# Kernel tuning notes

Measured on AMD Instinct MI355X. Metric: run time of the kernel, lower is better.

The kernel has to match this reference:

```python
import jax, jax.numpy as jnp
import numpy as np

H = 4096
L_CAND = 4

def setup_inputs() -> dict:
    key = jax.random.key(0)
    ks = jax.random.split(key, 8)
    s = 1.0 / np.sqrt(H)
    L = jax.random.uniform(ks[0], (L_CAND, H, H), minval=-s, maxval=s, dtype=jnp.float32)
    R = jax.random.uniform(ks[1], (L_CAND, H, H), minval=-s, maxval=s, dtype=jnp.float32)
    b = jnp.zeros((L_CAND, 1, H), dtype=jnp.float32)
    # candidate 3 is initialized to identity / zero bias in the torch module
    L = L.at[3].set(jnp.eye(H, dtype=jnp.float32))
    R = R.at[3].set(jnp.eye(H, dtype=jnp.float32))
    W_score = jax.random.uniform(ks[2], (H, 1), minval=-s, maxval=s, dtype=jnp.float32)
    x = jax.random.normal(ks[3], (1, H), dtype=jnp.float32)
    h_prev = jax.random.normal(ks[4], (1, H), dtype=jnp.float32)
    return {"x": x, "h_prev": h_prev, "L": L, "R": R, "b": b, "W_score": W_score}

def reference(x, h_prev, L, R, b, W_score):
    def score_mix(lst):
        # lst: [l, 1, H] candidates -> softmax-weighted mixture + argmax + margin
        s = jnp.einsum('lbh,ho->l', lst, W_score)          # [l]
        w = jax.nn.softmax(s)
        out = jnp.einsum('l,lbh->bh', w, lst)              # [1, H]
        top2 = jax.lax.top_k(s, 2)[0]
        return out, jnp.argmax(s), top2[0] - top2[1]

    mmL = lambda v: jnp.einsum('bh,lhk->lbk', v, L)        # batched [1,H]x[H,H] over l=4
    mmR = lambda v: jnp.einsum('bh,lhk->lbk', v, R)

    xL, hL, hR = mmL(x), mmL(h_prev), mmR(h_prev)
    z_1 = jax.nn.sigmoid(xL[0] + hR[0] + b[0])
    r   = jax.nn.sigmoid(xL[1] + hR[1] + b[1])
    z_2 = jax.nn.sigmoid(xL[0] + hR[0] + b[0])             # same as z_1 in source

    rh, i0, m0 = score_mix(hL * mmR(r) + b)
    h_tilde, i1, m1 = score_mix(jnp.tanh(xL + mmR(rh) + b))
    oneMinusZ1, i2, m2 = score_mix(1.0 - (mmR(z_1) + b))
    zh_tilde, i3, m3 = score_mix(mmL(h_tilde) * mmR(oneMinusZ1) + b)
    z2h, i4, m4 = score_mix(hL * mmR(z_2) + b)
    h_next, i5, m5 = score_mix(mmL(zh_tilde) + mmR(z2h) + b)

    G_structure = jnp.concatenate([jnp.array([0, 1, 0]),
                                   jnp.stack([i0, i1, i2, i3, i4, i5])])
    margins = jnp.stack([m0, m1, m2, m3, m4, m5])
    return h_next, G_structure, margins
```

## Files before the change

kernel.cpp:

```cpp
#include <hip/hip_runtime.h>
#include <hip/hip_fp16.h>

#define H 4096


template<int NV>
__global__ __launch_bounds__(256) void gemv_f32_k(const float* __restrict__ M,
                                                  const float* __restrict__ V0,
                                                  const float* __restrict__ V1,
                                                  float* __restrict__ out,
                                                  __half* __restrict__ M16) {
  int b = blockIdx.x;
  const int hc = b & 63;
  const int kt = (b >> 6) & 3;
  const int l  = b >> 8;
  const int tid = threadIdx.x;
  const int k0 = kt * 1024 + tid * 4;
  const int h0 = hc * 64;

  __shared__ float vs[NV * 64];
  if (tid < 64) vs[tid] = V0[h0 + tid];
  if (NV > 1 && tid >= 64 && tid < 128) vs[tid] = V1[h0 + tid - 64];
  __syncthreads();

  const size_t base = ((size_t)l * H + h0) * H + k0;
  const float* Mp = M + base;
  __half* M16p = M16 + base;

  float acc[NV][4];
#pragma unroll
  for (int v = 0; v < NV; ++v)
#pragma unroll
    for (int j = 0; j < 4; ++j) acc[v][j] = 0.0f;

#pragma unroll 2
  for (int hh = 0; hh < 64; ++hh) {
    float4 m = *reinterpret_cast<const float4*>(Mp + (size_t)hh * H);
    __half t[4] = {__float2half(m.x), __float2half(m.y),
                   __float2half(m.z), __float2half(m.w)};
    *reinterpret_cast<uint2*>(M16p + (size_t)hh * H) =
        *reinterpret_cast<const uint2*>(t);
#pragma unroll
    for (int v = 0; v < NV; ++v) {
      const float s = vs[v * 64 + hh];
      acc[v][0] = fmaf(s, m.x, acc[v][0]);
      acc[v][1] = fmaf(s, m.y, acc[v][1]);
      acc[v][2] = fmaf(s, m.z, acc[v][2]);
      acc[v][3] = fmaf(s, m.w, acc[v][3]);
    }
  }
#pragma unroll
  for (int v = 0; v < NV; ++v)
#pragma unroll
    for (int j = 0; j < 4; ++j)
      atomicAdd(out + ((size_t)(v * 3 + l)) * H + k0 + j, acc[v][j]);
}

template<int NV, bool MIX>
__global__ __launch_bounds__(256) void gemv_f16_k(
    const __half* __restrict__ M, const float* __restrict__ vecbase,
    const float* __restrict__ scores, int sbase,
    float* __restrict__ out, float* __restrict__ mixstore,
    int os0, int os1, int os2, float* __restrict__ dout) {
  int b = blockIdx.x;
  const int hc = b & 63;
  const int kt = (b >> 6) & 1;
  const int l  = b >> 7;
  const int tid = threadIdx.x;
  const int k0 = kt * 2048 + tid * 8;
  const int h0 = hc * 64;

  __shared__ float vs[NV * 64];
  if (MIX) {
    const bool storeblk = (l == 0 && kt == 0);
    if (tid < 64) {
#pragma unroll
      for (int v = 0; v < NV; ++v) {
        const float* sc = scores + (size_t)(sbase + v) * 4;
        float s0 = sc[0], s1 = sc[1], s2 = sc[2], s3 = sc[3];
        float mx = fmaxf(fmaxf(s0, s1), fmaxf(s2, s3));
        float e0 = expf(s0 - mx), e1 = expf(s1 - mx);
        float e2 = expf(s2 - mx), e3 = expf(s3 - mx);
        float inv = 1.0f / (e0 + e1 + e2 + e3);
        const float* cb = vecbase + (size_t)v * 4 * H + h0 + tid;
        float m = (e0 * cb[0] + e1 * cb[H] + e2 * cb[2 * H] + e3 * cb[3 * H]) * inv;
        vs[v * 64 + tid] = m;
        if (storeblk) mixstore[(size_t)v * H + h0 + tid] = m;
      }
    }
    if (storeblk && hc == 0 && tid == 0) {
      const int os[3] = {os0, os1, os2};
#pragma unroll
      for (int v = 0; v < NV; ++v) {
        const float* sc = scores + (size_t)(sbase + v) * 4;
        float s[4] = {sc[0], sc[1], sc[2], sc[3]};
        int idx = 0; float mx = s[0];
        for (int q = 1; q < 4; ++q) if (s[q] > mx) { mx = s[q]; idx = q; }
        float second = -1e30f;
        for (int q = 0; q < 4; ++q) if (q != idx && s[q] > second) second = s[q];
        dout[H + 3 + os[v]] = (float)idx;
        dout[H + 9 + os[v]] = mx - second;
      }
    }
  } else {
    for (int i = tid; i < NV * 64; i += 256)
      vs[i] = vecbase[(size_t)(i >> 6) * H + h0 + (i & 63)];
  }
  __syncthreads();

  const __half* Mp = M + ((size_t)l * H + h0) * H + k0;

  float acc[NV][8];
#pragma unroll
  for (int v = 0; v < NV; ++v)
#pragma unroll
    for (int j = 0; j < 8; ++j) acc[v][j] = 0.0f;

#pragma unroll 2
  for (int hh = 0; hh < 64; ++hh) {
    union { uint4 u; __half2 h2[4]; } cv;
    cv.u = *reinterpret_cast<const uint4*>(Mp + (size_t)hh * H);
    float fr[8];
#pragma unroll
    for (int j = 0; j < 4; ++j) {
      float2 t = __half22float2(cv.h2[j]);
      fr[2 * j] = t.x; fr[2 * j + 1] = t.y;
    }
#pragma unroll
    for (int v = 0; v < NV; ++v) {
      const float s = vs[v * 64 + hh];
#pragma unroll
      for (int j = 0; j < 8; ++j) acc[v][j] = fmaf(s, fr[j], acc[v][j]);
    }
  }
#pragma unroll
  for (int v = 0; v < NV; ++v)
#pragma unroll
    for (int j = 0; j < 8; ++j)
      atomicAdd(out + ((size_t)(v * 3 + l)) * H + k0 + j, acc[v][j]);
}

__device__ __forceinline__ float sigmoidf_(float x) {
  return 1.0f / (1.0f + expf(-x));
}

__global__ __launch_bounds__(256) void zr_k(float* __restrict__ f,
                                            const float* __restrict__ bias) {
  const int h = blockIdx.x * 256 + threadIdx.x;
  f[56 * H + h] = sigmoidf_(f[0 * H + h] + f[6 * H + h] + bias[h]);
  f[55 * H + h] = sigmoidf_(f[1 * H + h] + f[7 * H + h] + bias[H + h]);
}

template<int NW>
__device__ __forceinline__ void reduce_atomic(float* vals, float* sc, int tid) {
  __shared__ float red[4][NW];
  const int lane = tid & 63, wv = tid >> 6;
#pragma unroll
  for (int j = 0; j < NW; ++j) {
    float v = vals[j];
#pragma unroll
    for (int off = 32; off > 0; off >>= 1) v += __shfl_down(v, off);
    if (lane == 0) red[wv][j] = v;
  }
  __syncthreads();
  if (tid < NW)
    atomicAdd(sc + tid, red[0][tid] + red[1][tid] + red[2][tid] + red[3][tid]);
}

__global__ __launch_bounds__(256) void cs2_k(float* __restrict__ f,
                                             const float* __restrict__ hprev,
                                             const float* __restrict__ bias,
                                             const float* __restrict__ Ws) {
  const int h = blockIdx.x * 256 + threadIdx.x;
  const int tid = threadIdx.x;
  const float hp = hprev[h];
  const float r3 = f[55 * H + h], z3 = f[56 * H + h];
  const float ws = Ws[h];
  float crh[4], com[4], cz2[4];
#pragma unroll
  for (int l = 0; l < 3; ++l) {
    const float hl = f[(3 + l) * H + h];
    const float rr = f[(9 + l) * H + h];
    const float zz = f[(12 + l) * H + h];
    const float bl = bias[(size_t)l * H + h];
    crh[l] = fmaf(hl, rr, bl);
    com[l] = 1.0f - (zz + bl);
    cz2[l] = fmaf(hl, zz, bl);
  }
  {
    const float bl = bias[(size_t)3 * H + h];
    crh[3] = fmaf(hp, r3, bl);
    com[3] = 1.0f - (z3 + bl);
    cz2[3] = fmaf(hp, z3, bl);
  }
#pragma unroll
  for (int l = 0; l < 4; ++l) {
    f[(31 + l) * H + h] = crh[l];
    f[(35 + l) * H + h] = com[l];
    f[(39 + l) * H + h] = cz2[l];
  }
  float vals[12];
#pragma unroll
  for (int l = 0; l < 4; ++l) {
    vals[l]     = crh[l] * ws;
    vals[4 + l] = com[l] * ws;
    vals[8 + l] = cz2[l] * ws;
  }
  reduce_atomic<12>(vals, f + 30 * H, tid);
}

#define OP_MUL  0
#define OP_TANH 1
#define OP_ADD  2

template<int OP>
__global__ __launch_bounds__(256) void csx_k(const float* __restrict__ A,
                                             const float* __restrict__ A3,
                                             const float* __restrict__ B,
                                             const float* __restrict__ B3,
                                             const float* __restrict__ bias,
                                             const float* __restrict__ Ws,
                                             float* __restrict__ cand,
                                             float* __restrict__ sc) {
  const int h = blockIdx.x * 256 + threadIdx.x;
  const int tid = threadIdx.x;
  const float ws = Ws[h];
  float c[4];
#pragma unroll
  for (int l = 0; l < 4; ++l) {
    const float a = (l < 3) ? A[(size_t)l * H + h] : A3[h];
    const float b = (l < 3) ? B[(size_t)l * H + h] : B3[h];
    const float bl = bias[(size_t)l * H + h];
    if (OP == OP_MUL)  c[l] = fmaf(a, b, bl);
    if (OP == OP_TANH) c[l] = tanhf(a + b + bl);
    if (OP == OP_ADD)  c[l] = a + b + bl;
    cand[(size_t)l * H + h] = c[l];
  }
  float vals[4] = {c[0] * ws, c[1] * ws, c[2] * ws, c[3] * ws};
  reduce_atomic<4>(vals, sc, tid);
}

__global__ __launch_bounds__(256) void final_k(const float* __restrict__ f,
                                               float* __restrict__ dout) {
  const int h = blockIdx.x * 256 + threadIdx.x;
  const float* sc = f + 30 * H + 5 * 4;
  float s0 = sc[0], s1 = sc[1], s2 = sc[2], s3 = sc[3];
  float mx = fmaxf(fmaxf(s0, s1), fmaxf(s2, s3));
  float e0 = expf(s0 - mx), e1 = expf(s1 - mx);
  float e2 = expf(s2 - mx), e3 = expf(s3 - mx);
  float inv = 1.0f / (e0 + e1 + e2 + e3);
  const float* cb = f + 51 * H + h;
  dout[h] = (e0 * cb[0] + e1 * cb[H] + e2 * cb[2 * H] + e3 * cb[3 * H]) * inv;
  if (blockIdx.x == 0 && threadIdx.x == 0) {
    float s[4] = {s0, s1, s2, s3};
    int idx = 0; float m = s[0];
    for (int q = 1; q < 4; ++q) if (s[q] > m) { m = s[q]; idx = q; }
    float second = -1e30f;
    for (int q = 0; q < 4; ++q) if (q != idx && s[q] > second) second = s[q];
    dout[H + 0] = 0.f; dout[H + 1] = 1.f; dout[H + 2] = 0.f;
    dout[H + 3 + 5] = (float)idx;
    dout[H + 9 + 5] = m - second;
  }
}

extern "C" void kernel_launch(void* const* d_in, const int* in_sizes, int n_in,
                              void* d_out, int out_size, void* d_ws, size_t ws_size,
                              hipStream_t stream) {
  const float* x  = (const float*)d_in[0];
  const float* hp = (const float*)d_in[1];
  const float* L  = (const float*)d_in[2];
  const float* R  = (const float*)d_in[3];
  const float* bb = (const float*)d_in[4];
  const float* Ws = (const float*)d_in[5];
  float* out = (float*)d_out;

  __half* L16 = (__half*)d_ws;
  __half* R16 = L16 + (size_t)3 * H * H;
  float*  f   = (float*)(R16 + (size_t)3 * H * H);
  float*  sc  = f + 30 * H;

  hipMemsetAsync(f, 0, (size_t)31 * H * sizeof(float), stream);

  gemv_f32_k<2><<<768, 256, 0, stream>>>(L, x, hp, f, L16);
  gemv_f32_k<1><<<768, 256, 0, stream>>>(R, hp, nullptr, f + 6 * H, R16);

  zr_k<<<16, 256, 0, stream>>>(f, bb);

  gemv_f16_k<2, false><<<384, 256, 0, stream>>>(R16, f + 55 * H, nullptr, 0,
                                                f + 9 * H, nullptr, 0, 0, 0, nullptr);
  cs2_k<<<16, 256, 0, stream>>>(f, hp, bb, Ws);

  gemv_f16_k<3, true><<<384, 256, 0, stream>>>(R16, f + 31 * H, sc, 0,
                                               f + 15 * H, f + 57 * H, 0, 2, 4, out);
  csx_k<OP_TANH><<<16, 256, 0, stream>>>(f, x, f + 15 * H, f + 57 * H,
                                         bb, Ws, f + 43 * H, sc + 12);

  gemv_f16_k<1, true><<<384, 256, 0, stream>>>(L16, f + 43 * H, sc, 3,
                                               f + 24 * H, f + 60 * H, 1, 0, 0, out);
  csx_k<OP_MUL><<<16, 256, 0, stream>>>(f + 24 * H, f + 60 * H, f + 18 * H,
                                        f + 58 * H, bb, Ws, f + 47 * H, sc + 16);

  gemv_f16_k<1, true><<<384, 256, 0, stream>>>(L16, f + 47 * H, sc, 4,
                                               f + 27 * H, f + 61 * H, 3, 0, 0, out);
  csx_k<OP_ADD><<<16, 256, 0, stream>>>(f + 27 * H, f + 61 * H, f + 21 * H,
                                        f + 59 * H, bb, Ws, f + 51 * H, sc + 20);

  final_k<<<16, 256, 0, stream>>>(f, out);
}
```

Measured before the change: 796.6 us.

## Fuse all GRU stages into one persistent kernel with grid barriers

Replaces the sequence of gemv and elementwise launches with a single persistent kernel of 768 blocks that runs every stage, separated by a hierarchical atomic grid barrier. Workspace zeroing moves inside the kernel and tile shapes change (128-row fp32 tiles, 32-row fp16 tiles). The aim is to remove launch overhead and inter-kernel gaps. In exchange it relies on all blocks being co-resident, adds barrier spin costs, and doubles the atomic traffic in the fp16 phases.

```diff
diff --git a/kernel.cpp b/kernel.cpp
--- a/kernel.cpp
+++ b/kernel.cpp
@@ -4,23 +4,84 @@
 #define H 4096
 
 
+__device__ __forceinline__ float sigmoidf_(float x) {
+  return 1.0f / (1.0f + expf(-x));
+}
+
+__device__ __forceinline__ void soft4(const float* sc, float* w) {
+  float s0 = sc[0], s1 = sc[1], s2 = sc[2], s3 = sc[3];
+  float mx = fmaxf(fmaxf(s0, s1), fmaxf(s2, s3));
+  float e0 = expf(s0 - mx), e1 = expf(s1 - mx);
+  float e2 = expf(s2 - mx), e3 = expf(s3 - mx);
+  float inv = 1.0f / (e0 + e1 + e2 + e3);
+  w[0] = e0 * inv; w[1] = e1 * inv; w[2] = e2 * inv; w[3] = e3 * inv;
+}
+
+__device__ __forceinline__ void idxmargin(const float* sc, float* dout, int os) {
+  float s[4] = {sc[0], sc[1], sc[2], sc[3]};
+  int idx = 0; float mx = s[0];
+  for (int q = 1; q < 4; ++q) if (s[q] > mx) { mx = s[q]; idx = q; }
+  float second = -1e30f;
+  for (int q = 0; q < 4; ++q) if (q != idx && s[q] > second) second = s[q];
+  dout[H + 3 + os] = (float)idx;
+  dout[H + 9 + os] = mx - second;
+}
+
+__device__ __forceinline__ void gridbar(int* bar) {
+  __syncthreads();
+  __threadfence();
+  if (threadIdx.x == 0) {
+    int* gen  = bar;
+    int* root = bar + 16;
+    int* gcnt = bar + 32 + (blockIdx.x >> 6) * 16;
+    int g = __hip_atomic_load(gen, __ATOMIC_RELAXED, __HIP_MEMORY_SCOPE_AGENT);
+    bool done = false;
+    if (atomicAdd(gcnt, 1) == 63) {
+      atomicExch(gcnt, 0);
+      if (atomicAdd(root, 1) == 11) {
+        atomicExch(root, 0);
+        atomicAdd(gen, 1);
+        done = true;
+      }
+    }
+    if (!done) {
+      while (__hip_atomic_load(gen, __ATOMIC_RELAXED,
+                               __HIP_MEMORY_SCOPE_AGENT) == g)
+        __builtin_amdgcn_s_sleep(4);
+    }
+  }
+  __syncthreads();
+  __threadfence();
+}
+
+template<int NW>
+__device__ __forceinline__ void reduce_atomic(float* vals, float* scdst, int tid) {
+  __shared__ float red[4][12];
+  const int lane = tid & 63, wv = tid >> 6;
+#pragma unroll
+  for (int j = 0; j < NW; ++j) {
+    float v = vals[j];
+#pragma unroll
+    for (int off = 32; off > 0; off >>= 1) v += __shfl_down(v, off);
+    if (lane == 0) red[wv][j] = v;
+  }
+  __syncthreads();
+  if (tid < NW)
+    atomicAdd(scdst + tid, red[0][tid] + red[1][tid] + red[2][tid] + red[3][tid]);
+}
+
 template<int NV>
-__global__ __launch_bounds__(256) void gemv_f32_k(const float* __restrict__ M,
-                                                  const float* __restrict__ V0,
-                                                  const float* __restrict__ V1,
-                                                  float* __restrict__ out,
-                                                  __half* __restrict__ M16) {
-  int b = blockIdx.x;
-  const int hc = b & 63;
-  const int kt = (b >> 6) & 3;
-  const int l  = b >> 8;
+__device__ void phase_gemv32(const float* __restrict__ M,
+                             const float* __restrict__ V0,
+                             const float* __restrict__ V1,
+                             float* __restrict__ fout,
+                             __half* __restrict__ M16, int task, float* smem) {
+  const int hc = task & 31, kt = (task >> 5) & 3, l = task >> 7;
   const int tid = threadIdx.x;
   const int k0 = kt * 1024 + tid * 4;
-  const int h0 = hc * 64;
-
-  __shared__ float vs[NV * 64];
-  if (tid < 64) vs[tid] = V0[h0 + tid];
-  if (NV > 1 && tid >= 64 && tid < 128) vs[tid] = V1[h0 + tid - 64];
+  const int h0 = hc * 128;
+  if (tid < 128) smem[tid] = V0[h0 + tid];
+  else if (NV > 1) smem[tid] = V1[h0 + tid - 128];
   __syncthreads();
 
   const size_t base = ((size_t)l * H + h0) * H + k0;
@@ -33,8 +94,8 @@
 #pragma unroll
     for (int j = 0; j < 4; ++j) acc[v][j] = 0.0f;
 
-#pragma unroll 2
-  for (int hh = 0; hh < 64; ++hh) {
+#pragma unroll 4
+  for (int hh = 0; hh < 128; ++hh) {
     float4 m = *reinterpret_cast<const float4*>(Mp + (size_t)hh * H);
     __half t[4] = {__float2half(m.x), __float2half(m.y),
                    __float2half(m.z), __float2half(m.w)};
@@ -42,7 +103,7 @@
         *reinterpret_cast<const uint2*>(t);
 #pragma unroll
     for (int v = 0; v < NV; ++v) {
-      const float s = vs[v * 64 + hh];
+      const float s = smem[v * 128 + hh];
       acc[v][0] = fmaf(s, m.x, acc[v][0]);
       acc[v][1] = fmaf(s, m.y, acc[v][1]);
       acc[v][2] = fmaf(s, m.z, acc[v][2]);
@@ -53,71 +114,20 @@
   for (int v = 0; v < NV; ++v)
 #pragma unroll
     for (int j = 0; j < 4; ++j)
-      atomicAdd(out + ((size_t)(v * 3 + l)) * H + k0 + j, acc[v][j]);
-}
-
-template<int NV, bool MIX>
-__global__ __launch_bounds__(256) void gemv_f16_k(
-    const __half* __restrict__ M, const float* __restrict__ vecbase,
-    const float* __restrict__ scores, int sbase,
-    float* __restrict__ out, float* __restrict__ mixstore,
-    int os0, int os1, int os2, float* __restrict__ dout) {
-  int b = blockIdx.x;
-  const int hc = b & 63;
-  const int kt = (b >> 6) & 1;
-  const int l  = b >> 7;
-  const int tid = threadIdx.x;
-  const int k0 = kt * 2048 + tid * 8;
-  const int h0 = hc * 64;
-
-  __shared__ float vs[NV * 64];
-  if (MIX) {
-    const bool storeblk = (l == 0 && kt == 0);
-    if (tid < 64) {
-#pragma unroll
-      for (int v = 0; v < NV; ++v) {
-        const float* sc = scores + (size_t)(sbase + v) * 4;
-        float s0 = sc[0], s1 = sc[1], s2 = sc[2], s3 = sc[3];
-        float mx = fmaxf(fmaxf(s0, s1), fmaxf(s2, s3));
-        float e0 = expf(s0 - mx), e1 = expf(s1 - mx);
-        float e2 = expf(s2 - mx), e3 = expf(s3 - mx);
-        float inv = 1.0f / (e0 + e1 + e2 + e3);
-        const float* cb = vecbase + (size_t)v * 4 * H + h0 + tid;
-        float m = (e0 * cb[0] + e1 * cb[H] + e2 * cb[2 * H] + e3 * cb[3 * H]) * inv;
-        vs[v * 64 + tid] = m;
-        if (storeblk) mixstore[(size_t)v * H + h0 + tid] = m;
-      }
-    }
-    if (storeblk && hc == 0 && tid == 0) {
-      const int os[3] = {os0, os1, os2};
-#pragma unroll
-      for (int v = 0; v < NV; ++v) {
-        const float* sc = scores + (size_t)(sbase + v) * 4;
-        float s[4] = {sc[0], sc[1], sc[2], sc[3]};
-        int idx = 0; float mx = s[0];
-        for (int q = 1; q < 4; ++q) if (s[q] > mx) { mx = s[q]; idx = q; }
-        float second = -1e30f;
-        for (int q = 0; q < 4; ++q) if (q != idx && s[q] > second) second = s[q];
-        dout[H + 3 + os[v]] = (float)idx;
-        dout[H + 9 + os[v]] = mx - second;
-      }
-    }
-  } else {
-    for (int i = tid; i < NV * 64; i += 256)
-      vs[i] = vecbase[(size_t)(i >> 6) * H + h0 + (i & 63)];
-  }
-  __syncthreads();
-
-  const __half* Mp = M + ((size_t)l * H + h0) * H + k0;
-
+      atomicAdd(fout + (size_t)(v * 3 + l) * H + k0 + j, acc[v][j]);
+}
+
+template<int NV>
+__device__ void dot16(const __half* __restrict__ Mp, const float* __restrict__ vs,
+                      float* __restrict__ fout, int l, int k0) {
   float acc[NV][8];
 #pragma unroll
   for (int v = 0; v < NV; ++v)
 #pragma unroll
     for (int j = 0; j < 8; ++j) acc[v][j] = 0.0f;
 
-#pragma unroll 2
-  for (int hh = 0; hh < 64; ++hh) {
+#pragma unroll 4
+  for (int hh = 0; hh < 32; ++hh) {
     union { uint4 u; __half2 h2[4]; } cv;
     cv.u = *reinterpret_cast<const uint4*>(Mp + (size_t)hh * H);
     float fr[8];
@@ -128,7 +138,7 @@
     }
 #pragma unroll
     for (int v = 0; v < NV; ++v) {
-      const float s = vs[v * 64 + hh];
+      const float s = vs[v * 32 + hh];
 #pragma unroll
       for (int j = 0; j < 8; ++j) acc[v][j] = fmaf(s, fr[j], acc[v][j]);
     }
@@ -137,129 +147,191 @@
   for (int v = 0; v < NV; ++v)
 #pragma unroll
     for (int j = 0; j < 8; ++j)
-      atomicAdd(out + ((size_t)(v * 3 + l)) * H + k0 + j, acc[v][j]);
-}
-
-__device__ __forceinline__ float sigmoidf_(float x) {
-  return 1.0f / (1.0f + expf(-x));
-}
-
-__global__ __launch_bounds__(256) void zr_k(float* __restrict__ f,
-                                            const float* __restrict__ bias) {
-  const int h = blockIdx.x * 256 + threadIdx.x;
-  f[56 * H + h] = sigmoidf_(f[0 * H + h] + f[6 * H + h] + bias[h]);
-  f[55 * H + h] = sigmoidf_(f[1 * H + h] + f[7 * H + h] + bias[H + h]);
-}
-
-template<int NW>
-__device__ __forceinline__ void reduce_atomic(float* vals, float* sc, int tid) {
-  __shared__ float red[4][NW];
-  const int lane = tid & 63, wv = tid >> 6;
-#pragma unroll
-  for (int j = 0; j < NW; ++j) {
-    float v = vals[j];
-#pragma unroll
-    for (int off = 32; off > 0; off >>= 1) v += __shfl_down(v, off);
-    if (lane == 0) red[wv][j] = v;
-  }
-  __syncthreads();
-  if (tid < NW)
-    atomicAdd(sc + tid, red[0][tid] + red[1][tid] + red[2][tid] + red[3][tid]);
-}
-
-__global__ __launch_bounds__(256) void cs2_k(float* __restrict__ f,
-                                             const float* __restrict__ hprev,
-                                             const float* __restrict__ bias,
-                                             const float* __restrict__ Ws) {
-  const int h = blockIdx.x * 256 + threadIdx.x;
+      atomicAdd(fout + (size_t)(v * 3 + l) * H + k0 + j, acc[v][j]);
+}
+
+__global__ __launch_bounds__(256, 3) void mega_k(
+    const float* __restrict__ x, const float* __restrict__ hp,
+    const float* __restrict__ L, const float* __restrict__ R,
+    const float* __restrict__ bias, const float* __restrict__ Ws,
+    float* __restrict__ dout, __half* __restrict__ L16,
+    __half* __restrict__ R16, float* __restrict__ f, int* __restrict__ bar) {
+  __shared__ float smem[256];
+  const int b = blockIdx.x;
   const int tid = threadIdx.x;
-  const float hp = hprev[h];
-  const float r3 = f[55 * H + h], z3 = f[56 * H + h];
-  const float ws = Ws[h];
-  float crh[4], com[4], cz2[4];
-#pragma unroll
-  for (int l = 0; l < 3; ++l) {
-    const float hl = f[(3 + l) * H + h];
-    const float rr = f[(9 + l) * H + h];
-    const float zz = f[(12 + l) * H + h];
-    const float bl = bias[(size_t)l * H + h];
-    crh[l] = fmaf(hl, rr, bl);
-    com[l] = 1.0f - (zz + bl);
-    cz2[l] = fmaf(hl, zz, bl);
-  }
+  float* sc = f + 30 * H;
+
+  for (int i = b * 256 + tid; i < 31 * H; i += 768 * 256) f[i] = 0.0f;
+  gridbar(bar);
+
+  if (b < 384) phase_gemv32<2>(L, x, hp, f, L16, b, smem);
+  else         phase_gemv32<1>(R, hp, nullptr, f + 6 * H, R16, b - 384, smem);
+  gridbar(bar);
+
   {
-    const float bl = bias[(size_t)3 * H + h];
-    crh[3] = fmaf(hp, r3, bl);
-    com[3] = 1.0f - (z3 + bl);
-    cz2[3] = fmaf(hp, z3, bl);
-  }
-#pragma unroll
-  for (int l = 0; l < 4; ++l) {
-    f[(31 + l) * H + h] = crh[l];
-    f[(35 + l) * H + h] = com[l];
-    f[(39 + l) * H + h] = cz2[l];
-  }
-  float vals[12];
-#pragma unroll
-  for (int l = 0; l < 4; ++l) {
-    vals[l]     = crh[l] * ws;
-    vals[4 + l] = com[l] * ws;
-    vals[8 + l] = cz2[l] * ws;
-  }
-  reduce_atomic<12>(vals, f + 30 * H, tid);
-}
-
-#define OP_MUL  0
-#define OP_TANH 1
-#define OP_ADD  2
-
-template<int OP>
-__global__ __launch_bounds__(256) void csx_k(const float* __restrict__ A,
-                                             const float* __restrict__ A3,
-                                             const float* __restrict__ B,
-                                             const float* __restrict__ B3,
-                                             const float* __restrict__ bias,
-                                             const float* __restrict__ Ws,
-                                             float* __restrict__ cand,
-                                             float* __restrict__ sc) {
-  const int h = blockIdx.x * 256 + threadIdx.x;
-  const int tid = threadIdx.x;
-  const float ws = Ws[h];
-  float c[4];
-#pragma unroll
-  for (int l = 0; l < 4; ++l) {
-    const float a = (l < 3) ? A[(size_t)l * H + h] : A3[h];
-    const float b = (l < 3) ? B[(size_t)l * H + h] : B3[h];
-    const float bl = bias[(size_t)l * H + h];
-    if (OP == OP_MUL)  c[l] = fmaf(a, b, bl);
-    if (OP == OP_TANH) c[l] = tanhf(a + b + bl);
-    if (OP == OP_ADD)  c[l] = a + b + bl;
-    cand[(size_t)l * H + h] = c[l];
-  }
-  float vals[4] = {c[0] * ws, c[1] * ws, c[2] * ws, c[3] * ws};
-  reduce_atomic<4>(vals, sc, tid);
-}
-
-__global__ __launch_bounds__(256) void final_k(const float* __restrict__ f,
-                                               float* __restrict__ dout) {
-  const int h = blockIdx.x * 256 + threadIdx.x;
-  const float* sc = f + 30 * H + 5 * 4;
-  float s0 = sc[0], s1 = sc[1], s2 = sc[2], s3 = sc[3];
-  float mx = fmaxf(fmaxf(s0, s1), fmaxf(s2, s3));
-  float e0 = expf(s0 - mx), e1 = expf(s1 - mx);
-  float e2 = expf(s2 - mx), e3 = expf(s3 - mx);
-  float inv = 1.0f / (e0 + e1 + e2 + e3);
-  const float* cb = f + 51 * H + h;
-  dout[h] = (e0 * cb[0] + e1 * cb[H] + e2 * cb[2 * H] + e3 * cb[3 * H]) * inv;
-  if (blockIdx.x == 0 && threadIdx.x == 0) {
-    float s[4] = {s0, s1, s2, s3};
-    int idx = 0; float m = s[0];
-    for (int q = 1; q < 4; ++q) if (s[q] > m) { m = s[q]; idx = q; }
-    float second = -1e30f;
-    for (int q = 0; q < 4; ++q) if (q != idx && s[q] > second) second = s[q];
-    dout[H + 0] = 0.f; dout[H + 1] = 1.f; dout[H + 2] = 0.f;
-    dout[H + 3 + 5] = (float)idx;
-    dout[H + 9 + 5] = m - second;
+    const int hc = b & 127, kt = (b >> 7) & 1, l = b >> 8;
+    const int h0 = hc * 32, k0 = kt * 2048 + tid * 8;
+    if (tid < 32) {
+      int row = h0 + tid;
+      smem[tid]      = sigmoidf_(f[1 * H + row] + f[7 * H + row] + bias[H + row]);
+      smem[32 + tid] = sigmoidf_(f[0 * H + row] + f[6 * H + row] + bias[row]);
+    }
+    __syncthreads();
+    dot16<2>(R16 + ((size_t)l * H + h0) * H + k0, smem, f + 9 * H, l, k0);
+  }
+  gridbar(bar);
+
+  if (b < 16) {
+    const int h = b * 256 + tid;
+    const float hpv = hp[h];
+    const float z3 = sigmoidf_(f[0 * H + h] + f[6 * H + h] + bias[h]);
+    const float r3 = sigmoidf_(f[1 * H + h] + f[7 * H + h] + bias[H + h]);
+    const float ws = Ws[h];
+    float vals[12];
+#pragma unroll
+    for (int l = 0; l < 3; ++l) {
+      const float hl = f[(3 + l) * H + h], rr = f[(9 + l) * H + h],
+                  zz = f[(12 + l) * H + h];
+      const float bl = bias[(size_t)l * H + h];
+      float crh = fmaf(hl, rr, bl), com = 1.0f - (zz + bl), cz2 = fmaf(hl, zz, bl);
+      f[(size_t)(31 + l) * H + h] = crh;
+      f[(size_t)(35 + l) * H + h] = com;
+      f[(size_t)(39 + l) * H + h] = cz2;
+      vals[l] = crh * ws; vals[4 + l] = com * ws; vals[8 + l] = cz2 * ws;
+    }
+    {
+      const float bl = bias[(size_t)3 * H + h];
+      float crh = fmaf(hpv, r3, bl), com = 1.0f - (z3 + bl), cz2 = fmaf(hpv, z3, bl);
+      f[(size_t)34 * H + h] = crh;
+      f[(size_t)38 * H + h] = com;
+      f[(size_t)42 * H + h] = cz2;
+      vals[3] = crh * ws; vals[7] = com * ws; vals[11] = cz2 * ws;
+    }
+    reduce_atomic<12>(vals, sc, tid);
+  }
+  gridbar(bar);
+
+  {
+    const int hc = b & 127, kt = (b >> 7) & 1, l = b >> 8;
+    const int h0 = hc * 32, k0 = kt * 2048 + tid * 8;
+    const bool storeblk = (l == 0 && kt == 0);
+    if (tid < 32) {
+      int row = h0 + tid;
+#pragma unroll
+      for (int v = 0; v < 3; ++v) {
+        float w[4]; soft4(sc + v * 4, w);
+        const float* cb = f + (size_t)(31 + v * 4) * H + row;
+        float m = w[0] * cb[0] + w[1] * cb[H] + w[2] * cb[2 * H] + w[3] * cb[3 * H];
+        smem[v * 32 + tid] = m;
+        if (storeblk) f[(size_t)(57 + v) * H + row] = m;
+      }
+    }
+    if (storeblk && hc == 0 && tid == 0) {
+      idxmargin(sc + 0, dout, 0);
+      idxmargin(sc + 4, dout, 2);
+      idxmargin(sc + 8, dout, 4);
+    }
+    __syncthreads();
+    dot16<3>(R16 + ((size_t)l * H + h0) * H + k0, smem, f + 15 * H, l, k0);
+  }
+  gridbar(bar);
+
+  if (b < 16) {
+    const int h = b * 256 + tid;
+    const float ws = Ws[h];
+    float vals[4];
+#pragma unroll
+    for (int l = 0; l < 4; ++l) {
+      const float a  = (l < 3) ? f[(size_t)l * H + h] : x[h];
+      const float bv = (l < 3) ? f[(size_t)(15 + l) * H + h] : f[(size_t)57 * H + h];
+      const float bl = bias[(size_t)l * H + h];
+      float c = tanhf(a + bv + bl);
+      f[(size_t)(43 + l) * H + h] = c;
+      vals[l] = c * ws;
+    }
+    reduce_atomic<4>(vals, sc + 12, tid);
+  }
+  gridbar(bar);
+
+  {
+    const int hc = b & 127, kt = (b >> 7) & 1, l = b >> 8;
+    const int h0 = hc * 32, k0 = kt * 2048 + tid * 8;
+    const bool storeblk = (l == 0 && kt == 0);
+    if (tid < 32) {
+      int row = h0 + tid;
+      float w[4]; soft4(sc + 12, w);
+      const float* cb = f + (size_t)43 * H + row;
+      float m = w[0] * cb[0] + w[1] * cb[H] + w[2] * cb[2 * H] + w[3] * cb[3 * H];
+      smem[tid] = m;
+      if (storeblk) f[(size_t)60 * H + row] = m;
+    }
+    if (storeblk && hc == 0 && tid == 0) idxmargin(sc + 12, dout, 1);
+    __syncthreads();
+    dot16<1>(L16 + ((size_t)l * H + h0) * H + k0, smem, f + 24 * H, l, k0);
+  }
+  gridbar(bar);
+
+  if (b < 16) {
+    const int h = b * 256 + tid;
+    const float ws = Ws[h];
+    float vals[4];
+#pragma unroll
+    for (int l = 0; l < 4; ++l) {
+      const float a  = (l < 3) ? f[(size_t)(24 + l) * H + h] : f[(size_t)60 * H + h];
+      const float bv = (l < 3) ? f[(size_t)(18 + l) * H + h] : f[(size_t)58 * H + h];
+      const float bl = bias[(size_t)l * H + h];
+      float c = fmaf(a, bv, bl);
+      f[(size_t)(47 + l) * H + h] = c;
+      vals[l] = c * ws;
+    }
+    reduce_atomic<4>(vals, sc + 16, tid);
+  }
+  gridbar(bar);
+
+  {
+    const int hc = b & 127, kt = (b >> 7) & 1, l = b >> 8;
+    const int h0 = hc * 32, k0 = kt * 2048 + tid * 8;
+    const bool storeblk = (l == 0 && kt == 0);
+    if (tid < 32) {
+      int row = h0 + tid;
+      float w[4]; soft4(sc + 16, w);
+      const float* cb = f + (size_t)47 * H + row;
+      float m = w[0] * cb[0] + w[1] * cb[H] + w[2] * cb[2 * H] + w[3] * cb[3 * H];
+      smem[tid] = m;
+      if (storeblk) f[(size_t)61 * H + row] = m;
+    }
+    if (storeblk && hc == 0 && tid == 0) idxmargin(sc + 16, dout, 3);
+    __syncthreads();
+    dot16<1>(L16 + ((size_t)l * H + h0) * H + k0, smem, f + 27 * H, l, k0);
+  }
+  gridbar(bar);
+
+  if (b < 16) {
+    const int h = b * 256 + tid;
+    const float ws = Ws[h];
+    float vals[4];
+#pragma unroll
+    for (int l = 0; l < 4; ++l) {
+      const float a  = (l < 3) ? f[(size_t)(27 + l) * H + h] : f[(size_t)61 * H + h];
+      const float bv = (l < 3) ? f[(size_t)(21 + l) * H + h] : f[(size_t)59 * H + h];
+      const float bl = bias[(size_t)l * H + h];
+      float c = a + bv + bl;
+      f[(size_t)(51 + l) * H + h] = c;
+      vals[l] = c * ws;
+    }
+    reduce_atomic<4>(vals, sc + 20, tid);
+  }
+  gridbar(bar);
+
+  if (b < 16) {
+    const int h = b * 256 + tid;
+    float w[4]; soft4(sc + 20, w);
+    const float* cb = f + (size_t)51 * H + h;
+    dout[h] = w[0] * cb[0] + w[1] * cb[H] + w[2] * cb[2 * H] + w[3] * cb[3 * H];
+    if (b == 0 && tid == 0) {
+      dout[H + 0] = 0.f; dout[H + 1] = 1.f; dout[H + 2] = 0.f;
+      idxmargin(sc + 20, dout, 5);
+    }
   }
 }
 
@@ -277,33 +349,9 @@
   __half* L16 = (__half*)d_ws;
   __half* R16 = L16 + (size_t)3 * H * H;
   float*  f   = (float*)(R16 + (size_t)3 * H * H);
-  float*  sc  = f + 30 * H;
-
-  hipMemsetAsync(f, 0, (size_t)31 * H * sizeof(float), stream);
-
-  gemv_f32_k<2><<<768, 256, 0, stream>>>(L, x, hp, f, L16);
-  gemv_f32_k<1><<<768, 256, 0, stream>>>(R, hp, nullptr, f + 6 * H, R16);
-
-  zr_k<<<16, 256, 0, stream>>>(f, bb);
-
-  gemv_f16_k<2, false><<<384, 256, 0, stream>>>(R16, f + 55 * H, nullptr, 0,
-                                                f + 9 * H, nullptr, 0, 0, 0, nullptr);
-  cs2_k<<<16, 256, 0, stream>>>(f, hp, bb, Ws);
-
-  gemv_f16_k<3, true><<<384, 256, 0, stream>>>(R16, f + 31 * H, sc, 0,
-                                               f + 15 * H, f + 57 * H, 0, 2, 4, out);
-  csx_k<OP_TANH><<<16, 256, 0, stream>>>(f, x, f + 15 * H, f + 57 * H,
-                                         bb, Ws, f + 43 * H, sc + 12);
-
-  gemv_f16_k<1, true><<<384, 256, 0, stream>>>(L16, f + 43 * H, sc, 3,
-                                               f + 24 * H, f + 60 * H, 1, 0, 0, out);
-  csx_k<OP_MUL><<<16, 256, 0, stream>>>(f + 24 * H, f + 60 * H, f + 18 * H,
-                                        f + 58 * H, bb, Ws, f + 47 * H, sc + 16);
-
-  gemv_f16_k<1, true><<<384, 256, 0, stream>>>(L16, f + 47 * H, sc, 4,
-                                               f + 27 * H, f + 61 * H, 3, 0, 0, out);
-  csx_k<OP_ADD><<<16, 256, 0, stream>>>(f + 27 * H, f + 61 * H, f + 21 * H,
-                                        f + 59 * H, bb, Ws, f + 51 * H, sc + 20);
-
-  final_k<<<16, 256, 0, stream>>>(f, out);
-}
+  int*    bar = (int*)(f + 62 * H);
+
+  hipMemsetAsync(bar, 0, 256 * sizeof(int), stream);
+
+  mega_k<<<768, 256, 0, stream>>>(x, hp, L, R, bb, Ws, out, L16, R16, f, bar);
+}
```

New measurement: 1.875 ms. 2.35x slower.
